# Kernel tuning notes

Hardware: AMD Instinct MI355X
Metric: run time of the kernel (lower is better)

## Reference

```python
import jax, jax.numpy as jnp
import numpy as np
import math

B, S, F, R = 16, 2048, 512, 4
EPS = 1e-5

def setup_inputs() -> dict:
    key = jax.random.key(0)
    ks = jax.random.split(key, 8)
    s = 1.0 / math.sqrt(S)
    return {
        "x": jax.random.normal(ks[0], (B, S, F), dtype=jnp.float32),
        "Wq": jax.random.uniform(ks[1], (R, S), jnp.float32, -s, s),
        "bq": jnp.zeros((R,), jnp.float32),
        "Wk": jax.random.uniform(ks[2], (R, S), jnp.float32, -s, s),
        "bk": jnp.zeros((R,), jnp.float32),
        "Wv": jax.random.uniform(ks[3], (S, S), jnp.float32, -s, s),
        "bv": jnp.zeros((S,), jnp.float32),
        "ln_w": jnp.ones((S, F), jnp.float32),
        "ln_b": jnp.zeros((S, F), jnp.float32),
        "alpha": jnp.asarray(0.1, jnp.float32),
        "beta": jnp.asarray(0.1, jnp.float32),
    }

def reference(x, Wq, bq, Wk, bk, Wv, bv, ln_w, ln_b, alpha, beta):
    # LayerNorm over last two dims [S, F]
    mu = jnp.mean(x, axis=(1, 2), keepdims=True)
    var = jnp.mean(jnp.square(x - mu), axis=(1, 2), keepdims=True)
    x_norm = (x - mu) * jax.lax.rsqrt(var + EPS) * ln_w + ln_b
    x_t = jnp.swapaxes(x_norm, 1, 2)  # [B, F, S]
    Q = jnp.einsum('bfs,rs->bfr', x_t, Wq) + bq  # [B, F, R]
    K = jnp.einsum('bfs,rs->bfr', x_t, Wk) + bk  # [B, F, R]
    A = jnp.einsum('bfr,bgr->bfg', Q, K) / math.sqrt(R)  # [B, F, F]
    A = jax.nn.softmax(A, axis=-1)
    V = jnp.einsum('bfs,ts->bft', x_t, Wv) + bv  # [B, F, S]
    out = jnp.einsum('bfg,bgs->bfs', A, V)  # [B, F, S]
    # dropout in eval mode = identity
    out = x_t + alpha * out + V + beta * V
    return jnp.swapaxes(out, 1, 2)  # [B, S, F]
```

## Files before the change

### kernel.cpp

```cpp
#include <hip/hip_runtime.h>
#include <hip/hip_bf16.h>

#define NB 16
#define SS 2048
#define FF 512

typedef __bf16 bf16_t;
typedef __bf16 bf16x8 __attribute__((ext_vector_type(8)));
typedef __bf16 bf16x4 __attribute__((ext_vector_type(4)));
typedef float  f32x4  __attribute__((ext_vector_type(4)));

__global__ __launch_bounds__(256) void stats_kernel(const float* __restrict__ x,
                                                    float* __restrict__ partials) {
    const int b = blockIdx.y;
    const float* xb = x + ((size_t)b << 20) + (size_t)blockIdx.x * 16384;
    float s = 0.0f, ss = 0.0f;
#pragma unroll
    for (int i = 0; i < 16; ++i) {
        const float4 v = *(const float4*)&xb[(threadIdx.x + i * 256) * 4];
        s  += v.x + v.y + v.z + v.w;
        ss += v.x * v.x + v.y * v.y + v.z * v.z + v.w * v.w;
    }
#pragma unroll
    for (int off = 32; off > 0; off >>= 1) {
        s  += __shfl_down(s, off);
        ss += __shfl_down(ss, off);
    }
    __shared__ float ps[4], pss[4];
    const int w = threadIdx.x >> 6, lane = threadIdx.x & 63;
    if (lane == 0) { ps[w] = s; pss[w] = ss; }
    __syncthreads();
    if (threadIdx.x == 0) {
        partials[b * 64 + blockIdx.x]        = ps[0] + ps[1] + ps[2] + ps[3];
        partials[1024 + b * 64 + blockIdx.x] = pss[0] + pss[1] + pss[2] + pss[3];
    }
}

__global__ __launch_bounds__(256) void finalize_stats(const float* __restrict__ partials,
                                                      float* __restrict__ musig) {
    const int tid = threadIdx.x;
    const int b = tid >> 4, i = tid & 15;
    float s = 0.f, ss = 0.f;
#pragma unroll
    for (int j = 0; j < 4; ++j) {
        s  += partials[b * 64 + i * 4 + j];
        ss += partials[1024 + b * 64 + i * 4 + j];
    }
#pragma unroll
    for (int off = 8; off > 0; off >>= 1) {
        s  += __shfl_xor(s, off);
        ss += __shfl_xor(ss, off);
    }
    if (i == 0) {
        const float inv_n = 1.0f / 1048576.0f;
        const float mu  = s * inv_n;
        const float var = ss * inv_n - mu * mu;
        musig[b]      = mu;
        musig[16 + b] = rsqrtf(var + 1e-5f);
    }
}

__global__ __launch_bounds__(256) void ynorm_kernel(const float* __restrict__ x,
                                                    const float* __restrict__ lw,
                                                    const float* __restrict__ lb,
                                                    const float* __restrict__ musig,
                                                    bf16_t* __restrict__ Y) {
    __shared__ bf16_t t[32][36];
    const int b = blockIdx.z;
    const int f0 = blockIdx.x * 32, s0 = blockIdx.y * 32;
    const float mu = musig[b], rs = musig[16 + b];
    const int tid = threadIdx.x;
    {
        const int s_loc = tid >> 3, c4 = (tid & 7) * 4;
        const size_t idx = (size_t)(s0 + s_loc) * FF + f0 + c4;
        const float4 xv = *(const float4*)&x[((size_t)b << 20) + idx];
        const float4 wv = *(const float4*)&lw[idx];
        const float4 bv = *(const float4*)&lb[idx];
        t[s_loc][c4 + 0] = (bf16_t)((xv.x - mu) * rs * wv.x + bv.x);
        t[s_loc][c4 + 1] = (bf16_t)((xv.y - mu) * rs * wv.y + bv.y);
        t[s_loc][c4 + 2] = (bf16_t)((xv.z - mu) * rs * wv.z + bv.z);
        t[s_loc][c4 + 3] = (bf16_t)((xv.w - mu) * rs * wv.w + bv.w);
    }
    __syncthreads();
    {
        const int f_loc = tid >> 3, s4 = (tid & 7) * 4;
        bf16x4 o;
        o[0] = t[s4 + 0][f_loc];
        o[1] = t[s4 + 1][f_loc];
        o[2] = t[s4 + 2][f_loc];
        o[3] = t[s4 + 3][f_loc];
        *(bf16x4*)&Y[((size_t)b << 20) + (size_t)(f0 + f_loc) * SS + s0 + s4] = o;
    }
}

__global__ __launch_bounds__(256) void cast_wv(const float* __restrict__ Wv,
                                               bf16_t* __restrict__ Wvb) {
    const size_t i = ((size_t)blockIdx.x * 256 + threadIdx.x) * 4;
    const float4 v = *(const float4*)&Wv[i];
    bf16x4 o;
    o[0] = (bf16_t)v.x; o[1] = (bf16_t)v.y; o[2] = (bf16_t)v.z; o[3] = (bf16_t)v.w;
    *(bf16x4*)&Wvb[i] = o;
}

__global__ __launch_bounds__(256) void qk_kernel(const bf16_t* __restrict__ Y,
                                                 const float* __restrict__ Wq,
                                                 const float* __restrict__ bq,
                                                 const float* __restrict__ Wk,
                                                 const float* __restrict__ bk,
                                                 float* __restrict__ Qo,
                                                 float* __restrict__ Ko) {
    const int w = threadIdx.x >> 6, lane = threadIdx.x & 63;
    const int row = blockIdx.x * 4 + w;
    const bf16_t* y = Y + (size_t)row * SS;
    float qa[4] = {0.f, 0.f, 0.f, 0.f}, ka[4] = {0.f, 0.f, 0.f, 0.f};
#pragma unroll
    for (int c = 0; c < 4; ++c) {
        const int s = c * 512 + lane * 8;
        const bf16x8 yv = *(const bf16x8*)&y[s];
        float yf[8];
#pragma unroll
        for (int j = 0; j < 8; ++j) yf[j] = (float)yv[j];
#pragma unroll
        for (int r = 0; r < 4; ++r) {
            const float4 a0 = *(const float4*)&Wq[r * SS + s];
            const float4 a1 = *(const float4*)&Wq[r * SS + s + 4];
            const float4 c0 = *(const float4*)&Wk[r * SS + s];
            const float4 c1 = *(const float4*)&Wk[r * SS + s + 4];
            qa[r] += yf[0]*a0.x + yf[1]*a0.y + yf[2]*a0.z + yf[3]*a0.w
                   + yf[4]*a1.x + yf[5]*a1.y + yf[6]*a1.z + yf[7]*a1.w;
            ka[r] += yf[0]*c0.x + yf[1]*c0.y + yf[2]*c0.z + yf[3]*c0.w
                   + yf[4]*c1.x + yf[5]*c1.y + yf[6]*c1.z + yf[7]*c1.w;
        }
    }
#pragma unroll
    for (int off = 32; off > 0; off >>= 1) {
#pragma unroll
        for (int r = 0; r < 4; ++r) {
            qa[r] += __shfl_down(qa[r], off);
            ka[r] += __shfl_down(ka[r], off);
        }
    }
    if (lane == 0) {
#pragma unroll
        for (int r = 0; r < 4; ++r) {
            Qo[(size_t)row * 4 + r] = qa[r] + bq[r];
            Ko[(size_t)row * 4 + r] = ka[r] + bk[r];
        }
    }
}

__global__ __launch_bounds__(256) void softmax_kernel(const float* __restrict__ Qo,
                                                      const float* __restrict__ Ko,
                                                      bf16_t* __restrict__ Aout) {
    const int w = threadIdx.x >> 6, lane = threadIdx.x & 63;
    const int row = blockIdx.x * 4 + w;
    const int b = row >> 9;
    const float4 q = *(const float4*)&Qo[(size_t)row * 4];
    const float* kb = Ko + (size_t)b * FF * 4;
    float sc[8];
#pragma unroll
    for (int j = 0; j < 8; ++j) {
        const float4 kv = *(const float4*)&kb[(lane * 8 + j) * 4];
        sc[j] = (q.x*kv.x + q.y*kv.y + q.z*kv.z + q.w*kv.w) * 0.5f;
    }
    float mx = sc[0];
#pragma unroll
    for (int j = 1; j < 8; ++j) mx = fmaxf(mx, sc[j]);
#pragma unroll
    for (int off = 32; off > 0; off >>= 1) mx = fmaxf(mx, __shfl_xor(mx, off));
    float sum = 0.f;
#pragma unroll
    for (int j = 0; j < 8; ++j) { sc[j] = __expf(sc[j] - mx); sum += sc[j]; }
#pragma unroll
    for (int off = 32; off > 0; off >>= 1) sum += __shfl_xor(sum, off);
    const float inv = 1.0f / sum;
    bf16x8 o;
#pragma unroll
    for (int j = 0; j < 8; ++j) o[j] = (bf16_t)(sc[j] * inv);
    *(bf16x8*)&Aout[(size_t)row * FF + lane * 8] = o;
}

template<bool FUSE>
__global__ __launch_bounds__(512, 2) void gemm_nt_pipe(
        const bf16_t* __restrict__ Abase, long long strideA, int lda,
        const bf16_t* __restrict__ Bbase, long long strideB, int ldb,
        bf16_t* __restrict__ Cbase, long long strideC, int ldc,
        int NTILES, const float* __restrict__ bias_m,
        const float* __restrict__ xp, const float* __restrict__ lwp,
        const float* __restrict__ lbp, const float* __restrict__ musig,
        const float* __restrict__ alphap, const float* __restrict__ betap,
        float* __restrict__ outp) {
    __shared__ __align__(16) bf16_t As[2][16384];
    __shared__ __align__(16) bf16_t Bs[2][16384];
    const int tid = threadIdx.x;
    const int w = tid >> 6, lane = tid & 63;

    const int nchunk = gridDim.x >> 3;
    const int wgid = (blockIdx.x & 7) * nchunk + (blockIdx.x >> 3);
    const int bz = wgid >> 4;
    const int rem = wgid & 15;
    const int m0 = (rem & 7) * 256, n0 = (rem >> 3) * 256;

    const bf16_t* A = Abase + (size_t)bz * (size_t)strideA;
    const bf16_t* B = Bbase + (size_t)bz * (size_t)strideB;
    bf16_t* C = Cbase + (size_t)bz * (size_t)strideC;
    const int wm = w >> 2, wn = w & 3;

    const int rr0 = (w * 2 + 0) * 16 + (lane >> 2);
    const int rr1 = (w * 2 + 1) * 16 + (lane >> 2);
    const int sw0 = ((lane & 3) ^ ((rr0 >> 1) & 3)) * 8;
    const int sw1 = ((lane & 3) ^ ((rr1 >> 1) & 3)) * 8;
    const bf16_t* gA0 = A + (size_t)(m0 + rr0) * lda + sw0;
    const bf16_t* gA1 = A + (size_t)(m0 + rr1) * lda + sw1;
    const bf16_t* gB0 = B + (size_t)(n0 + rr0) * ldb + sw0;
    const bf16_t* gB1 = B + (size_t)(n0 + rr1) * ldb + sw1;
    const int d0 = (w * 2 + 0) * 512;
    const int d1 = (w * 2 + 1) * 512;

#define STA(bi, h, ko) do {                                                          \
    __builtin_amdgcn_global_load_lds(                                                \
        (const __attribute__((address_space(1))) unsigned int*)(gA0 + (ko) + (h)*32),\
        (__attribute__((address_space(3))) unsigned int*)&As[bi][(h)*8192 + d0], 16, 0, 0); \
    __builtin_amdgcn_global_load_lds(                                                \
        (const __attribute__((address_space(1))) unsigned int*)(gA1 + (ko) + (h)*32),\
        (__attribute__((address_space(3))) unsigned int*)&As[bi][(h)*8192 + d1], 16, 0, 0); \
} while (0)
#define STB(bi, h, ko) do {                                                          \
    __builtin_amdgcn_global_load_lds(                                                \
        (const __attribute__((address_space(1))) unsigned int*)(gB0 + (ko) + (h)*32),\
        (__attribute__((address_space(3))) unsigned int*)&Bs[bi][(h)*8192 + d0], 16, 0, 0); \
    __builtin_amdgcn_global_load_lds(                                                \
        (const __attribute__((address_space(1))) unsigned int*)(gB1 + (ko) + (h)*32),\
        (__attribute__((address_space(3))) unsigned int*)&Bs[bi][(h)*8192 + d1], 16, 0, 0); \
} while (0)

    const int cs = lane >> 4;
    int offA[2][8], offB[2][4];
#pragma unroll
    for (int kk = 0; kk < 2; ++kk) {
#pragma unroll
        for (int mt = 0; mt < 8; ++mt) {
            const int r = wm * 128 + mt * 16 + (lane & 15);
            offA[kk][mt] = kk * 8192 + r * 32 + ((cs ^ ((r >> 1) & 3)) << 3);
        }
#pragma unroll
        for (int nt = 0; nt < 4; ++nt) {
            const int r = wn * 64 + nt * 16 + (lane & 15);
            offB[kk][nt] = kk * 8192 + r * 32 + ((cs ^ ((r >> 1) & 3)) << 3);
        }
    }

#define RD_A(dst, base, kk, mh) do { _Pragma("unroll")                        \
    for (int i = 0; i < 4; ++i) dst[i] = *(const bf16x8*)&(base)[offA[kk][(mh)*4 + i]]; } while (0)
#define RD_B(dst, base, kk) do { _Pragma("unroll")                            \
    for (int i = 0; i < 4; ++i) dst[i] = *(const bf16x8*)&(base)[offB[kk][i]]; } while (0)
#define MFMA16X(af, bfr, mh) do { _Pragma("unroll")                           \
    for (int i = 0; i < 4; ++i) { _Pragma("unroll")                           \
        for (int nt = 0; nt < 4; ++nt)                                        \
            acc[(mh)*4 + i][nt] = __builtin_amdgcn_mfma_f32_16x16x32_bf16(    \
                af[i], bfr[nt], acc[(mh)*4 + i][nt], 0, 0, 0); } } while (0)
#define VMC(n) asm volatile("s_waitcnt vmcnt(" #n ")" ::: "memory")
#define HBAR  __builtin_amdgcn_s_barrier()
#define LGKM(n) do { asm volatile("s_waitcnt lgkmcnt(" #n ")" ::: "memory");  \
                     __builtin_amdgcn_sched_barrier(0); } while (0)
#define SBAR  __builtin_amdgcn_sched_barrier(0)
#define PRIO1 __builtin_amdgcn_s_setprio(1)
#define PRIO0 __builtin_amdgcn_s_setprio(0)

    f32x4 acc[8][4] = {};
    bf16x8 afA[4], afB[4], bfrA[4], bfrB[4];
    const int mask = NTILES - 1;

    STA(0, 0, 0); STB(0, 0, 0); STA(0, 1, 0); STB(0, 1, 0);
    VMC(4); HBAR;
    RD_A(afA, As[0], 0, 0); RD_B(bfrA, Bs[0], 0);

    for (int t = 0; t < NTILES; ++t) {
        const int cur = t & 1, oth = cur ^ 1;
        const int ko = ((t + 1) & mask) * 64;
        const bf16_t* as  = As[cur];
        const bf16_t* bs  = Bs[cur];
        const bf16_t* asn = As[oth];
        const bf16_t* bsn = Bs[oth];
        RD_A(afB, as, 0, 1); SBAR;
        STA(oth, 0, ko); SBAR;
        LGKM(4);
        PRIO1; MFMA16X(afA, bfrA, 0); PRIO0; SBAR;
        VMC(2); HBAR;
        RD_A(afA, as, 1, 0); RD_B(bfrB, bs, 1); SBAR;
        STB(oth, 0, ko); SBAR;
        LGKM(8);
        PRIO1; MFMA16X(afB, bfrA, 1); PRIO0; SBAR;
        RD_A(afB, as, 1, 1); SBAR;
        STA(oth, 1, ko); SBAR;
        LGKM(4);
        PRIO1; MFMA16X(afA, bfrB, 0); PRIO0; SBAR;
        VMC(2); HBAR;
        RD_A(afA, asn, 0, 0); RD_B(bfrA, bsn, 0); SBAR;
        STB(oth, 1, ko); SBAR;
        LGKM(8);
        PRIO1; MFMA16X(afB, bfrB, 1); PRIO0; SBAR;
    }
#undef STA
#undef STB
#undef RD_A
#undef RD_B
#undef MFMA16X
#undef VMC
#undef HBAR
#undef LGKM
#undef SBAR
#undef PRIO1
#undef PRIO0

    if constexpr (!FUSE) {
#pragma unroll
        for (int mt = 0; mt < 8; ++mt) {
#pragma unroll
            for (int r = 0; r < 4; ++r) {
                const int row = m0 + wm * 128 + mt * 16 + ((lane >> 4) << 2) + r;
                const float bm = bias_m ? bias_m[row] : 0.0f;
#pragma unroll
                for (int nt = 0; nt < 4; ++nt) {
                    const int col = n0 + wn * 64 + nt * 16 + (lane & 15);
                    C[(size_t)row * ldc + col] = (bf16_t)(acc[mt][nt][r] + bm);
                }
            }
        }
    } else {
        asm volatile("s_waitcnt vmcnt(0) lgkmcnt(0)" ::: "memory");
        __syncthreads();
        float* lsc = (float*)&As[0][0];
        const float mu = musig[bz], rs = musig[16 + bz];
        const float alpha = alphap[0];
        const float onepb = 1.0f + betap[0];
        const float* xb = xp + ((size_t)bz << 20);
        float* ob = outp + ((size_t)bz << 20);
        const int lrow = wm * 16 + ((lane >> 4) << 2);
        const int lcol = wn * 64 + (lane & 15);
        const int gr = tid >> 4;
        const int gc = (tid & 15) * 16;
        for (int mt = 0; mt < 8; ++mt) {
#pragma unroll
            for (int r = 0; r < 4; ++r)
#pragma unroll
                for (int nt = 0; nt < 4; ++nt)
                    lsc[(lrow + r) * 256 + lcol + nt * 16] = acc[mt][nt][r];
            __syncthreads();
            const int grow = m0 + (gr >> 4) * 128 + mt * 16 + (gr & 15);
            const size_t idx = (size_t)grow * FF + n0 + gc;
#pragma unroll
            for (int j = 0; j < 4; ++j) {
                const float4 av = *(const float4*)&lsc[gr * 256 + gc + j * 4];
                const float4 xv = *(const float4*)&xb[idx + j * 4];
                const float4 wv = *(const float4*)&lwp[idx + j * 4];
                const float4 bv4 = *(const float4*)&lbp[idx + j * 4];
                const bf16x4 vv = *(const bf16x4*)&A[idx + j * 4];
                float4 o;
                o.x = (xv.x - mu) * rs * wv.x + bv4.x + alpha * av.x + onepb * (float)vv[0];
                o.y = (xv.y - mu) * rs * wv.y + bv4.y + alpha * av.y + onepb * (float)vv[1];
                o.z = (xv.z - mu) * rs * wv.z + bv4.z + alpha * av.z + onepb * (float)vv[2];
                o.w = (xv.w - mu) * rs * wv.w + bv4.w + alpha * av.w + onepb * (float)vv[3];
                *(float4*)&ob[idx + j * 4] = o;
            }
            __syncthreads();
        }
    }
}

extern "C" void kernel_launch(void* const* d_in, const int* in_sizes, int n_in,
                              void* d_out, int out_size, void* d_ws, size_t ws_size,
                              hipStream_t stream) {
    const float* x   = (const float*)d_in[0];
    const float* Wq  = (const float*)d_in[1];
    const float* bq  = (const float*)d_in[2];
    const float* Wk  = (const float*)d_in[3];
    const float* bk  = (const float*)d_in[4];
    const float* Wv  = (const float*)d_in[5];
    const float* bv  = (const float*)d_in[6];
    const float* lw  = (const float*)d_in[7];
    const float* lb  = (const float*)d_in[8];
    const float* alp = (const float*)d_in[9];
    const float* bet = (const float*)d_in[10];
    float* out = (float*)d_out;

    char* ws = (char*)d_ws;
    float*  musig = (float*)(ws + 128);
    float*  Qo    = (float*)(ws + 256);
    float*  Ko    = (float*)(ws + 256 + 131072);
    bf16_t* Wvb   = (bf16_t*)(ws + 262400);
    bf16_t* Asm   = (bf16_t*)(ws + 8651008);
    float*  partials = (float*)(ws + 8651008);
    bf16_t* Vt    = (bf16_t*)(ws + 17039616);
    bf16_t* Y     = (bf16_t*)(ws + 50594048);

    stats_kernel<<<dim3(64, 16), 256, 0, stream>>>(x, partials);
    finalize_stats<<<1, 256, 0, stream>>>(partials, musig);
    cast_wv<<<4096, 256, 0, stream>>>(Wv, Wvb);
    ynorm_kernel<<<dim3(16, 64, 16), 256, 0, stream>>>(x, lw, lb, musig, Y);
    qk_kernel<<<2048, 256, 0, stream>>>(Y, Wq, bq, Wk, bk, Qo, Ko);
    softmax_kernel<<<2048, 256, 0, stream>>>(Qo, Ko, Asm);
    gemm_nt_pipe<false><<<256, 512, 0, stream>>>(
        Wvb, 0, SS, Y, 1 << 20, SS, Vt, 1 << 20, FF, 32, bv,
        nullptr, nullptr, nullptr, nullptr, nullptr, nullptr, nullptr);
    gemm_nt_pipe<true><<<256, 512, 0, stream>>>(
        Vt, 1 << 20, FF, Asm, FF * FF, FF, nullptr, 0, FF, 8, nullptr,
        x, lw, lb, musig, alp, bet, out);
}
```

Before: 192.3 us.

## Cache normalized x in bf16 and double-buffer the fused GEMM epilogue

The ynorm kernel now also writes a row-major bf16 copy of the normalized input. When the workspace is large enough, the final GEMM epilogue reads that copy instead of re-reading fp32 x, ln_w and ln_b and recomputing the LayerNorm. The epilogue also double-buffers the LDS staging of accumulators so the next tile's scatter overlaps the current tile's global loads, and it issues the V and x loads as wider vectors. In exchange the ynorm kernel does an extra 32MB write, and the residual x term loses precision because it is now rounded to bf16.

```diff
diff --git a/kernel.cpp b/kernel.cpp
--- a/kernel.cpp
+++ b/kernel.cpp
@@ -64,7 +64,8 @@
                                                     const float* __restrict__ lw,
                                                     const float* __restrict__ lb,
                                                     const float* __restrict__ musig,
-                                                    bf16_t* __restrict__ Y) {
+                                                    bf16_t* __restrict__ Y,
+                                                    bf16_t* __restrict__ Xn) {
     __shared__ bf16_t t[32][36];
     const int b = blockIdx.z;
     const int f0 = blockIdx.x * 32, s0 = blockIdx.y * 32;
@@ -76,10 +77,16 @@
         const float4 xv = *(const float4*)&x[((size_t)b << 20) + idx];
         const float4 wv = *(const float4*)&lw[idx];
         const float4 bv = *(const float4*)&lb[idx];
-        t[s_loc][c4 + 0] = (bf16_t)((xv.x - mu) * rs * wv.x + bv.x);
-        t[s_loc][c4 + 1] = (bf16_t)((xv.y - mu) * rs * wv.y + bv.y);
-        t[s_loc][c4 + 2] = (bf16_t)((xv.z - mu) * rs * wv.z + bv.z);
-        t[s_loc][c4 + 3] = (bf16_t)((xv.w - mu) * rs * wv.w + bv.w);
+        bf16x4 o;
+        o[0] = (bf16_t)((xv.x - mu) * rs * wv.x + bv.x);
+        o[1] = (bf16_t)((xv.y - mu) * rs * wv.y + bv.y);
+        o[2] = (bf16_t)((xv.z - mu) * rs * wv.z + bv.z);
+        o[3] = (bf16_t)((xv.w - mu) * rs * wv.w + bv.w);
+        t[s_loc][c4 + 0] = o[0];
+        t[s_loc][c4 + 1] = o[1];
+        t[s_loc][c4 + 2] = o[2];
+        t[s_loc][c4 + 3] = o[3];
+        if (Xn) *(bf16x4*)&Xn[((size_t)b << 20) + idx] = o;
     }
     __syncthreads();
     {
@@ -180,14 +187,15 @@
     *(bf16x8*)&Aout[(size_t)row * FF + lane * 8] = o;
 }
 
-template<bool FUSE>
-__global__ __launch_bounds__(512, 2) void gemm_nt_pipe(
+template<int EPI>
+__device__ __forceinline__ void gemm_impl(
         const bf16_t* __restrict__ Abase, long long strideA, int lda,
         const bf16_t* __restrict__ Bbase, long long strideB, int ldb,
         bf16_t* __restrict__ Cbase, long long strideC, int ldc,
         int NTILES, const float* __restrict__ bias_m,
         const float* __restrict__ xp, const float* __restrict__ lwp,
-        const float* __restrict__ lbp, const float* __restrict__ musig,
+        const float* __restrict__ lbp, const bf16_t* __restrict__ xnp,
+        const float* __restrict__ musig,
         const float* __restrict__ alphap, const float* __restrict__ betap,
         float* __restrict__ outp) {
     __shared__ __align__(16) bf16_t As[2][16384];
@@ -313,7 +321,7 @@
 #undef PRIO1
 #undef PRIO0
 
-    if constexpr (!FUSE) {
+    if constexpr (EPI == 0) {
 #pragma unroll
         for (int mt = 0; mt < 8; ++mt) {
 #pragma unroll
@@ -330,42 +338,106 @@
     } else {
         asm volatile("s_waitcnt vmcnt(0) lgkmcnt(0)" ::: "memory");
         __syncthreads();
-        float* lsc = (float*)&As[0][0];
-        const float mu = musig[bz], rs = musig[16 + bz];
+        float* lsc0 = (float*)&As[0][0];
+        float* lsc1 = (float*)&As[1][0];
         const float alpha = alphap[0];
         const float onepb = 1.0f + betap[0];
-        const float* xb = xp + ((size_t)bz << 20);
+        float mu = 0.f, rs = 0.f;
+        if constexpr (EPI == 1) { mu = musig[bz]; rs = musig[16 + bz]; }
+        const float* xb = (EPI == 1) ? xp + ((size_t)bz << 20) : nullptr;
+        const bf16_t* xnb = (EPI == 2) ? xnp + ((size_t)bz << 20) : nullptr;
         float* ob = outp + ((size_t)bz << 20);
         const int lrow = wm * 16 + ((lane >> 4) << 2);
         const int lcol = wn * 64 + (lane & 15);
         const int gr = tid >> 4;
         const int gc = (tid & 15) * 16;
+#define SCAT(mt, bank) do { _Pragma("unroll")                                 \
+    for (int r = 0; r < 4; ++r) { _Pragma("unroll")                           \
+        for (int nt = 0; nt < 4; ++nt)                                        \
+            (bank)[(lrow + r) * 256 + lcol + nt * 16] = acc[mt][nt][r]; } } while (0)
+        SCAT(0, lsc0);
+        __syncthreads();
+#pragma unroll
         for (int mt = 0; mt < 8; ++mt) {
-#pragma unroll
-            for (int r = 0; r < 4; ++r)
-#pragma unroll
-                for (int nt = 0; nt < 4; ++nt)
-                    lsc[(lrow + r) * 256 + lcol + nt * 16] = acc[mt][nt][r];
-            __syncthreads();
+            float* bank  = (mt & 1) ? lsc1 : lsc0;
+            float* nbank = (mt & 1) ? lsc0 : lsc1;
             const int grow = m0 + (gr >> 4) * 128 + mt * 16 + (gr & 15);
             const size_t idx = (size_t)grow * FF + n0 + gc;
+            const bf16x8 vt0 = *(const bf16x8*)&A[(size_t)grow * lda + n0 + gc];
+            const bf16x8 vt1 = *(const bf16x8*)&A[(size_t)grow * lda + n0 + gc + 8];
+            bf16x8 xn0, xn1;
+            float4 xv[4], wv[4], bv4[4];
+            if constexpr (EPI == 2) {
+                xn0 = *(const bf16x8*)&xnb[idx];
+                xn1 = *(const bf16x8*)&xnb[idx + 8];
+            } else {
+#pragma unroll
+                for (int j = 0; j < 4; ++j) {
+                    xv[j]  = *(const float4*)&xb[idx + j * 4];
+                    wv[j]  = *(const float4*)&lwp[idx + j * 4];
+                    bv4[j] = *(const float4*)&lbp[idx + j * 4];
+                }
+            }
+            if (mt < 7) {
+                switch (mt + 1) {
+                    case 1: SCAT(1, nbank); break;
+                    case 2: SCAT(2, nbank); break;
+                    case 3: SCAT(3, nbank); break;
+                    case 4: SCAT(4, nbank); break;
+                    case 5: SCAT(5, nbank); break;
+                    case 6: SCAT(6, nbank); break;
+                    case 7: SCAT(7, nbank); break;
+                }
+            }
 #pragma unroll
             for (int j = 0; j < 4; ++j) {
-                const float4 av = *(const float4*)&lsc[gr * 256 + gc + j * 4];
-                const float4 xv = *(const float4*)&xb[idx + j * 4];
-                const float4 wv = *(const float4*)&lwp[idx + j * 4];
-                const float4 bv4 = *(const float4*)&lbp[idx + j * 4];
-                const bf16x4 vv = *(const bf16x4*)&A[idx + j * 4];
+                const float4 av = *(const float4*)&bank[gr * 256 + gc + j * 4];
                 float4 o;
-                o.x = (xv.x - mu) * rs * wv.x + bv4.x + alpha * av.x + onepb * (float)vv[0];
-                o.y = (xv.y - mu) * rs * wv.y + bv4.y + alpha * av.y + onepb * (float)vv[1];
-                o.z = (xv.z - mu) * rs * wv.z + bv4.z + alpha * av.z + onepb * (float)vv[2];
-                o.w = (xv.w - mu) * rs * wv.w + bv4.w + alpha * av.w + onepb * (float)vv[3];
+                if constexpr (EPI == 2) {
+                    const int e = (j & 1) * 4;
+                    const bf16x8& xs = (j < 2) ? xn0 : xn1;
+                    const bf16x8& vs = (j < 2) ? vt0 : vt1;
+                    o.x = (float)xs[e + 0] + alpha * av.x + onepb * (float)vs[e + 0];
+                    o.y = (float)xs[e + 1] + alpha * av.y + onepb * (float)vs[e + 1];
+                    o.z = (float)xs[e + 2] + alpha * av.z + onepb * (float)vs[e + 2];
+                    o.w = (float)xs[e + 3] + alpha * av.w + onepb * (float)vs[e + 3];
+                } else {
+                    const int e = (j & 1) * 4;
+                    const bf16x8& vs = (j < 2) ? vt0 : vt1;
+                    o.x = (xv[j].x - mu) * rs * wv[j].x + bv4[j].x + alpha * av.x + onepb * (float)vs[e + 0];
+                    o.y = (xv[j].y - mu) * rs * wv[j].y + bv4[j].y + alpha * av.y + onepb * (float)vs[e + 1];
+                    o.z = (xv[j].z - mu) * rs * wv[j].z + bv4[j].z + alpha * av.z + onepb * (float)vs[e + 2];
+                    o.w = (xv[j].w - mu) * rs * wv[j].w + bv4[j].w + alpha * av.w + onepb * (float)vs[e + 3];
+                }
                 *(float4*)&ob[idx + j * 4] = o;
             }
             __syncthreads();
         }
-    }
+#undef SCAT
+    }
+}
+
+__global__ __launch_bounds__(512, 2) void g1_mm(
+        const bf16_t* A, long long sA, int lda, const bf16_t* B, long long sB, int ldb,
+        bf16_t* C, long long sC, int ldc, int NT, const float* bias_m) {
+    gemm_impl<0>(A, sA, lda, B, sB, ldb, C, sC, ldc, NT, bias_m,
+                 nullptr, nullptr, nullptr, nullptr, nullptr, nullptr, nullptr, nullptr);
+}
+
+__global__ __launch_bounds__(512, 2) void g2_mm_full(
+        const bf16_t* A, long long sA, int lda, const bf16_t* B, long long sB, int ldb,
+        int NT, const float* xp, const float* lwp, const float* lbp,
+        const float* musig, const float* alphap, const float* betap, float* outp) {
+    gemm_impl<1>(A, sA, lda, B, sB, ldb, nullptr, 0, FF, NT, nullptr,
+                 xp, lwp, lbp, nullptr, musig, alphap, betap, outp);
+}
+
+__global__ __launch_bounds__(512, 2) void g2_mm_lite(
+        const bf16_t* A, long long sA, int lda, const bf16_t* B, long long sB, int ldb,
+        int NT, const bf16_t* xnp,
+        const float* musig, const float* alphap, const float* betap, float* outp) {
+    gemm_impl<2>(A, sA, lda, B, sB, ldb, nullptr, 0, FF, NT, nullptr,
+                 nullptr, nullptr, nullptr, xnp, musig, alphap, betap, outp);
 }
 
 extern "C" void kernel_launch(void* const* d_in, const int* in_sizes, int n_in,
@@ -393,17 +465,22 @@
     float*  partials = (float*)(ws + 8651008);
     bf16_t* Vt    = (bf16_t*)(ws + 17039616);
     bf16_t* Y     = (bf16_t*)(ws + 50594048);
+    bf16_t* Xn    = (bf16_t*)(ws + 84148480);
+    const bool lite = ws_size >= (size_t)117702912;
 
     stats_kernel<<<dim3(64, 16), 256, 0, stream>>>(x, partials);
     finalize_stats<<<1, 256, 0, stream>>>(partials, musig);
     cast_wv<<<4096, 256, 0, stream>>>(Wv, Wvb);
-    ynorm_kernel<<<dim3(16, 64, 16), 256, 0, stream>>>(x, lw, lb, musig, Y);
+    ynorm_kernel<<<dim3(16, 64, 16), 256, 0, stream>>>(x, lw, lb, musig, Y,
+                                                       lite ? Xn : (bf16_t*)nullptr);
     qk_kernel<<<2048, 256, 0, stream>>>(Y, Wq, bq, Wk, bk, Qo, Ko);
     softmax_kernel<<<2048, 256, 0, stream>>>(Qo, Ko, Asm);
-    gemm_nt_pipe<false><<<256, 512, 0, stream>>>(
-        Wvb, 0, SS, Y, 1 << 20, SS, Vt, 1 << 20, FF, 32, bv,
-        nullptr, nullptr, nullptr, nullptr, nullptr, nullptr, nullptr);
-    gemm_nt_pipe<true><<<256, 512, 0, stream>>>(
-        Vt, 1 << 20, FF, Asm, FF * FF, FF, nullptr, 0, FF, 8, nullptr,
-        x, lw, lb, musig, alp, bet, out);
-}
+    g1_mm<<<256, 512, 0, stream>>>(Wvb, 0, SS, Y, 1 << 20, SS, Vt, 1 << 20, FF, 32, bv);
+    if (lite) {
+        g2_mm_lite<<<256, 512, 0, stream>>>(Vt, 1 << 20, FF, Asm, FF * FF, FF, 8,
+                                            Xn, musig, alp, bet, out);
+    } else {
+        g2_mm_full<<<256, 512, 0, stream>>>(Vt, 1 << 20, FF, Asm, FF * FF, FF, 8,
+                                            x, lw, lb, musig, alp, bet, out);
+    }
+}
```

Measured after the change: 181.8 us. -5.4%, faster.
